# Kernel tuning notes

Hardware: AMD Instinct MI355X
Metric: run time of the kernel (lower is better)

Reference implementation:

```python
import math
import jax, jax.numpy as jnp
import numpy as np

D = 256      # embedding_dim (= internal_dim, downsample_rate 1)
H = 8        # num_heads
HD = D // H  # head_dim = 32
NTC = 16     # num_text_classes
NIMG = 4096  # image tokens (64x64)
N = NIMG + NTC
B = 2
NKE = 64     # num_k_exclude_rope


def _rope(x, freqs):
    # x: (b, h, n, c); freqs: (n, c//2, 2) = (cos, sin) of complex rotary factors
    b, h, n, c = x.shape
    xp = x.reshape(b, h, n, c // 2, 2)
    cos, sin = freqs[..., 0], freqs[..., 1]
    xr, xi = xp[..., 0], xp[..., 1]
    out_r = xr * cos - xi * sin
    out_i = xr * sin + xi * cos
    return jnp.stack([out_r, out_i], axis=-1).reshape(b, h, n, c)


def _sep_heads(x):
    b, n, c = x.shape
    return x.reshape(b, n, H, c // H).transpose(0, 2, 1, 3)  # (b,h,n,hd)


def setup_inputs() -> dict:
    key = jax.random.key(0)
    ks = jax.random.split(key, 14)
    s = 0.02
    # rotary factors: unit-norm cos/sin pairs
    ang_img = jax.random.uniform(ks[3], (NIMG, HD // 2)) * (2.0 * np.pi)
    ang_txt = jax.random.uniform(ks[4], (NTC, HD // 2)) * (2.0 * np.pi)
    return {
        "q": jax.random.normal(ks[0], (B, N, D), dtype=jnp.float32),
        "k": jax.random.normal(ks[1], (B, N, D), dtype=jnp.float32),
        "v": jax.random.normal(ks[2], (B, N, D), dtype=jnp.float32),
        "freqs_cis_img": jnp.stack([jnp.cos(ang_img), jnp.sin(ang_img)], axis=-1),
        "freqs_cis_txt": jnp.stack([jnp.cos(ang_txt), jnp.sin(ang_txt)], axis=-1),
        "Wq": jax.random.normal(ks[5], (D, D), dtype=jnp.float32) * s,
        "bq": jnp.zeros((D,), dtype=jnp.float32),
        "Wk": jax.random.normal(ks[6], (D, D), dtype=jnp.float32) * s,
        "bk": jnp.zeros((D,), dtype=jnp.float32),
        "Wv": jax.random.normal(ks[7], (D, D), dtype=jnp.float32) * s,
        "bv": jnp.zeros((D,), dtype=jnp.float32),
        "Wo": jax.random.normal(ks[8], (D, D), dtype=jnp.float32) * s,
        "bo": jnp.zeros((D,), dtype=jnp.float32),
        "num_k_exclude_rope": NKE,
    }


def reference(q, k, v, freqs_cis_img, freqs_cis_txt,
              Wq, bq, Wk, bk, Wv, bv, Wo, bo, num_k_exclude_rope):
    q = q @ Wq.T + bq
    k = k @ Wk.T + bk
    v = v @ Wv.T + bv
    q = _sep_heads(q)  # (b,h,n,hd)
    k = _sep_heads(k)
    v = _sep_heads(v)

    # split tokens into image / text regions, apply RoPE separately
    q_img, q_txt = q[:, :, :-NTC, :], q[:, :, -NTC:, :]
    k_img, k_txt = k[:, :, :-NTC, :], k[:, :, -NTC:, :]
    q_img = _rope(q_img, freqs_cis_img)
    k_img = _rope(k_img, freqs_cis_img)
    q_txt = _rope(q_txt, freqs_cis_txt)
    k_txt = _rope(k_txt, freqs_cis_txt)
    q = jnp.concatenate([q_img, q_txt], axis=-2)
    k = jnp.concatenate([k_img, k_txt], axis=-2)

    scale = 1.0 / math.sqrt(HD)
    nke = num_k_exclude_rope
    if nke > 0:
        k_td, k_mem = k[:, :, :-nke, :], k[:, :, -nke:, :]
        v_td, v_mem = v[:, :, :-nke, :], v[:, :, -nke:, :]
        attn = jax.nn.softmax(jnp.einsum('bhqd,bhkd->bhqk', q, k_td) * scale, axis=-1)
        out = jnp.einsum('bhqk,bhkd->bhqd', attn, v_td)
        attn_m = jax.nn.softmax(jnp.einsum('bhqd,bhkd->bhqk', q, k_mem) * scale, axis=-1)
        out = out + jnp.einsum('bhqk,bhkd->bhqd', attn_m, v_mem)
    else:
        attn = jax.nn.softmax(jnp.einsum('bhqd,bhkd->bhqk', q, k) * scale, axis=-1)
        out = jnp.einsum('bhqk,bhkd->bhqd', attn, v)

    b, h, n, hd = out.shape
    out = out.transpose(0, 2, 1, 3).reshape(b, n, h * hd)
    return out @ Wo.T + bo
```

## Files before the change

kernel.cpp:

```cpp
#include <hip/hip_runtime.h>
#include <hip/hip_bf16.h>

#define BN    4112
#define NKR   4160
#define BNP   4160
#define BB    2
#define HH    8
#define NIMG_ 4096
#define NMAIN 4048
#define MROWS 8224
#define QSCALE 0.25505402f

typedef __attribute__((ext_vector_type(8))) short short8;
typedef __attribute__((ext_vector_type(4))) float f32x4;

__device__ __forceinline__ unsigned short f2bs(float x) { return __bfloat16_as_ushort(__float2bfloat16(x)); }
__device__ __forceinline__ unsigned pkbf(float a, float b) {
    __hip_bfloat162 h = __float22bfloat162_rn(make_float2(a, b));
    unsigned u; __builtin_memcpy(&u, &h, 4); return u;
}
__device__ __forceinline__ float fexp2(float x) {
#if __has_builtin(__builtin_amdgcn_exp2f)
    return __builtin_amdgcn_exp2f(x);
#else
    return exp2f(x);
#endif
}

__global__ __launch_bounds__(256)
void qkv_mfma(const float* __restrict__ Aq, const float* __restrict__ Ak, const float* __restrict__ Av,
              const float* __restrict__ Wq, const float* __restrict__ Wk, const float* __restrict__ Wv,
              const float* __restrict__ bq, const float* __restrict__ bk, const float* __restrict__ bv,
              short* __restrict__ Qr, short* __restrict__ Kr, short* __restrict__ Vt,
              const float* __restrict__ fimg, const float* __restrict__ ftxt)
{
    __shared__ __align__(16) short Ws[2][64][72];
    __shared__ __align__(16) short Ds[2][64][72];

    const int mode = blockIdx.z;
    const float* A    = (mode == 0) ? Aq : (mode == 1) ? Ak : Av;
    const float* W    = (mode == 0) ? Wq : (mode == 1) ? Wk : Wv;
    const float* bias = (mode == 0) ? bq : (mode == 1) ? bk : bv;

    const int t    = threadIdx.x;
    const int wave = t >> 6, lane = t & 63, q16 = lane & 15, quad = lane >> 4;
    const int f0 = blockIdx.x * 64;
    const int m0 = blockIdx.y * 64;
    const int sr = t >> 2, sc = (t & 3) * 16;
    const int arow = m0 + sr;
    const bool aval = arow < MROWS;
    const float* wp = W + (size_t)(f0 + sr) * 256 + sc;
    const float* ap = A + (size_t)(aval ? arow : 0) * 256 + sc;

    f32x4 acc[4] = {{0,0,0,0},{0,0,0,0},{0,0,0,0},{0,0,0,0}};

    uint4 wr0, wr1, dr0, dr1;
    {
        float4 a0 = *(const float4*)(wp),     a1 = *(const float4*)(wp + 4);
        float4 a2 = *(const float4*)(wp + 8), a3 = *(const float4*)(wp + 12);
        wr0 = uint4{pkbf(a0.x,a0.y), pkbf(a0.z,a0.w), pkbf(a1.x,a1.y), pkbf(a1.z,a1.w)};
        wr1 = uint4{pkbf(a2.x,a2.y), pkbf(a2.z,a2.w), pkbf(a3.x,a3.y), pkbf(a3.z,a3.w)};
        a0 = *(const float4*)(ap);     a1 = *(const float4*)(ap + 4);
        a2 = *(const float4*)(ap + 8); a3 = *(const float4*)(ap + 12);
        dr0 = uint4{pkbf(a0.x,a0.y), pkbf(a0.z,a0.w), pkbf(a1.x,a1.y), pkbf(a1.z,a1.w)};
        dr1 = uint4{pkbf(a2.x,a2.y), pkbf(a2.z,a2.w), pkbf(a3.x,a3.y), pkbf(a3.z,a3.w)};
    }
    *(uint4*)&Ws[0][sr][sc] = wr0; *(uint4*)&Ws[0][sr][sc + 8] = wr1;
    *(uint4*)&Ds[0][sr][sc] = dr0; *(uint4*)&Ds[0][sr][sc + 8] = dr1;
    __syncthreads();

    #pragma unroll
    for (int ki = 0; ki < 4; ++ki) {
        const int buf = ki & 1;
        if (ki < 3) {
            const int k1 = (ki + 1) * 64;
            float4 a0 = *(const float4*)(wp + k1),     a1 = *(const float4*)(wp + k1 + 4);
            float4 a2 = *(const float4*)(wp + k1 + 8), a3 = *(const float4*)(wp + k1 + 12);
            wr0 = uint4{pkbf(a0.x,a0.y), pkbf(a0.z,a0.w), pkbf(a1.x,a1.y), pkbf(a1.z,a1.w)};
            wr1 = uint4{pkbf(a2.x,a2.y), pkbf(a2.z,a2.w), pkbf(a3.x,a3.y), pkbf(a3.z,a3.w)};
            a0 = *(const float4*)(ap + k1);     a1 = *(const float4*)(ap + k1 + 4);
            a2 = *(const float4*)(ap + k1 + 8); a3 = *(const float4*)(ap + k1 + 12);
            dr0 = uint4{pkbf(a0.x,a0.y), pkbf(a0.z,a0.w), pkbf(a1.x,a1.y), pkbf(a1.z,a1.w)};
            dr1 = uint4{pkbf(a2.x,a2.y), pkbf(a2.z,a2.w), pkbf(a3.x,a3.y), pkbf(a3.z,a3.w)};
        }
        #pragma unroll
        for (int ks = 0; ks < 2; ++ks) {
            const short8 af = *(const short8*)&Ws[buf][wave * 16 + q16][ks * 32 + quad * 8];
            #pragma unroll
            for (int ct = 0; ct < 4; ++ct) {
                const short8 bf = *(const short8*)&Ds[buf][ct * 16 + q16][ks * 32 + quad * 8];
                acc[ct] = __builtin_amdgcn_mfma_f32_16x16x32_bf16(af, bf, acc[ct], 0, 0, 0);
            }
        }
        if (ki < 3) {
            *(uint4*)&Ws[buf ^ 1][sr][sc] = wr0; *(uint4*)&Ws[buf ^ 1][sr][sc + 8] = wr1;
            *(uint4*)&Ds[buf ^ 1][sr][sc] = dr0; *(uint4*)&Ds[buf ^ 1][sr][sc + 8] = dr1;
            __syncthreads();
        }
    }

    const int fbase = f0 + wave * 16 + quad * 4;
    const float4 bb = *(const float4*)(bias + fbase);
    float vs[4][4];
    #pragma unroll
    for (int ct = 0; ct < 4; ++ct) {
        int n = m0 + ct * 16 + q16;
        float v0 = acc[ct][0] + bb.x, v1 = acc[ct][1] + bb.y;
        float v2 = acc[ct][2] + bb.z, v3 = acc[ct][3] + bb.w;
        int b  = (n >= BN) ? 1 : 0;
        int nb = n - b * BN;
        if (mode < 2) {
            int j0 = (fbase & 31) >> 1;
            const float* fr = (nb < NIMG_) ? (fimg + ((size_t)nb * 16 + j0) * 2)
                                           : (ftxt + ((size_t)(nb - NIMG_) * 16 + j0) * 2);
            float4 cs = *(const float4*)fr;
            float r0 = v0 * cs.x - v1 * cs.y, i0 = v0 * cs.y + v1 * cs.x;
            float r1 = v2 * cs.z - v3 * cs.w, i1 = v2 * cs.w + v3 * cs.z;
            v0 = r0; v1 = i0; v2 = r1; v3 = i1;
        }
        if (mode == 2) {
            vs[ct][0] = v0; vs[ct][1] = v1; vs[ct][2] = v2; vs[ct][3] = v3;
            continue;
        }
        if (n >= MROWS) continue;
        const int h = (fbase >> 5) & 7, hd = fbase & 31;
        if (mode == 0) {
            unsigned short* op = (unsigned short*)Qr + (((size_t)(b * HH + h) * BN + nb) * 32 + hd);
            *(uint2*)op = uint2{pkbf(v0 * QSCALE, v1 * QSCALE), pkbf(v2 * QSCALE, v3 * QSCALE)};
        } else {
            int nk = nb + ((nb >= NMAIN) ? 48 : 0);
            unsigned short* op = (unsigned short*)Kr + (((size_t)(b * HH + h) * NKR + nk) * 32 + hd);
            *(uint2*)op = uint2{pkbf(v0, v1), pkbf(v2, v3)};
        }
    }

    if (mode == 2) {
        short (*Tr)[72] = Ds[0];
        const int fl = wave * 16 + quad * 4;
        #pragma unroll
        for (int ct = 0; ct < 4; ++ct) {
            const int nl = ct * 16 + q16;
            Tr[fl + 0][nl] = (short)f2bs(vs[ct][0]);
            Tr[fl + 1][nl] = (short)f2bs(vs[ct][1]);
            Tr[fl + 2][nl] = (short)f2bs(vs[ct][2]);
            Tr[fl + 3][nl] = (short)f2bs(vs[ct][3]);
        }
        __syncthreads();
        const int h0 = (f0 >> 5) & 7;
        #pragma unroll
        for (int ii = 0; ii < 2; ++ii) {
            const int r  = ii * 32 + (t >> 3);
            const int c8 = (t & 7) * 8;
            const int ng = m0 + c8;
            if (ng < MROWS) {
                uint4 val = *(const uint4*)&Tr[r][c8];
                int b  = (ng >= BN) ? 1 : 0;
                int nb = ng - b * BN;
                int nk = nb + ((nb >= NMAIN) ? 48 : 0);
                int h  = h0 + (r >> 5), hd = r & 31;
                unsigned short* op = (unsigned short*)Vt + ((size_t)(b * HH + h) * 32 + hd) * BNP + nk;
                *(uint4*)op = val;
            }
        }
    }

    if (blockIdx.x == 0 && blockIdx.y < 16 && t < 192) {
        const int bh = blockIdx.y;
        if (mode == 1) {
            short* base = Kr + (size_t)bh * NKR * 32 + (size_t)NMAIN * 32;
            *(uint4*)(base + t * 8) = uint4{0u, 0u, 0u, 0u};
        } else if (mode == 2) {
            short* base = Vt + (size_t)bh * 32 * BNP + (size_t)(t / 6) * BNP + NMAIN + (t % 6) * 8;
            *(uint4*)base = uint4{0u, 0u, 0u, 0u};
        }
    }
}

__global__ __launch_bounds__(512, 8)
void attn_mfma(const short* __restrict__ Qr, const short* __restrict__ Kr,
               const short* __restrict__ Vt, unsigned short* __restrict__ AO)
{
    __shared__ __align__(16) short Ks[2][2][64][40];
    __shared__ __align__(16) short Vs[2][2][32][72];

    const int t    = threadIdx.x;
    const int wave = t >> 6, lane = t & 63, q16 = lane & 15, quad = lane >> 4;
    const int grp  = wave >> 2, w4 = wave & 3;
    const int bh = blockIdx.y;
    const int q  = blockIdx.x * 64 + w4 * 16 + q16;
    const int qc = (q < BN) ? q : (BN - 1);
    const short8 qf = *(const short8*)(Qr + ((size_t)bh * BN + qc) * 32 + quad * 8);

    f32x4 oA0 = {0,0,0,0}, oA1 = {0,0,0,0}, oB0 = {0,0,0,0}, oB1 = {0,0,0,0};
    float LA = 0.f, LB = 0.f;

    const int tg = t & 255;
    const int kr = tg >> 2, kc = tg & 3;
    const int vr = tg >> 3, vc = tg & 7;
    const short* kg = Kr + (size_t)bh * NKR * 32 + (size_t)grp * 65536 + (size_t)kr * 32 + kc * 8;
    const short* vg = Vt + (size_t)bh * 32 * BNP + (size_t)vr * BNP + grp * 2048
                         + (vc >> 2) * 32 + (vc & 3) * 4;
    const int ntiles = 32 + grp;

    auto tile = [&](int buf, f32x4& o0, f32x4& o1, float& L) {
        float lsum = 0.f;
        #pragma unroll
        for (int g = 0; g < 2; ++g) {
            const short8 kf0 = *(const short8*)&Ks[grp][buf][(2*g)     * 16 + q16][quad * 8];
            const short8 kf1 = *(const short8*)&Ks[grp][buf][(2*g + 1) * 16 + q16][quad * 8];
            f32x4 z = {0,0,0,0};
            f32x4 s0 = __builtin_amdgcn_mfma_f32_16x16x32_bf16(kf0, qf, z, 0, 0, 0);
            f32x4 s1 = __builtin_amdgcn_mfma_f32_16x16x32_bf16(kf1, qf, z, 0, 0, 0);
            float p0 = fexp2(s0[0]), p1 = fexp2(s0[1]), p2 = fexp2(s0[2]), p3 = fexp2(s0[3]);
            float p4 = fexp2(s1[0]), p5 = fexp2(s1[1]), p6 = fexp2(s1[2]), p7 = fexp2(s1[3]);
            lsum += ((p0 + p1) + (p2 + p3)) + ((p4 + p5) + (p6 + p7));
            uint4 pbu = uint4{pkbf(p0, p1), pkbf(p2, p3), pkbf(p4, p5), pkbf(p6, p7)};
            short8 pb; __builtin_memcpy(&pb, &pbu, 16);
            const short8 vf = *(const short8*)&Vs[grp][buf][q16][g * 32 + quad * 8];
            o0 = __builtin_amdgcn_mfma_f32_16x16x32_bf16(vf, pb, o0, 0, 0, 0);
            const short8 vb = *(const short8*)&Vs[grp][buf][16 + q16][g * 32 + quad * 8];
            o1 = __builtin_amdgcn_mfma_f32_16x16x32_bf16(vb, pb, o1, 0, 0, 0);
        }
        L += lsum;
    };

    *(uint4*)&Ks[grp][0][kr][kc * 8] = *(const uint4*)(kg);
    {
        uint2 va = *(const uint2*)(vg);
        uint2 vbr = *(const uint2*)(vg + 16);
        *(uint4*)&Vs[grp][0][vr][vc * 8] = uint4{va.x, va.y, vbr.x, vbr.y};
    }
    __syncthreads();

    for (int it = 0; it < 33; ++it) {
        const int buf = it & 1;
        uint4 kreg; uint2 vreg0, vreg1;
        const bool pre = (it + 1) < ntiles;
        if (pre) {
            kreg  = *(const uint4*)(kg + (size_t)(it + 1) * 2048);
            vreg0 = *(const uint2*)(vg + (it + 1) * 64);
            vreg1 = *(const uint2*)(vg + (it + 1) * 64 + 16);
        }
        if (it < ntiles) {
            if (grp == 0) tile(buf, oA0, oA1, LA);
            else if (it < 32) tile(buf, oA0, oA1, LA);
            else              tile(buf, oB0, oB1, LB);
        }
        if (pre) {
            *(uint4*)&Ks[grp][buf ^ 1][kr][kc * 8] = kreg;
            *(uint4*)&Vs[grp][buf ^ 1][vr][vc * 8] = uint4{vreg0.x, vreg0.y, vreg1.x, vreg1.y};
        }
        __syncthreads();
    }

    LA += __shfl_xor(LA, 16); LA += __shfl_xor(LA, 32);
    LB += __shfl_xor(LB, 16); LB += __shfl_xor(LB, 32);

    float* ex = (float*)&Ks[0][0][0][0];
    const int slot = (w4 * 64 + lane) * 12;
    if (grp == 0) {
        *(f32x4*)(ex + slot)     = oA0;
        *(f32x4*)(ex + slot + 4) = oA1;
        ex[slot + 8] = LA;
    }
    __syncthreads();

    if (grp == 1 && q < BN) {
        f32x4 a0 = *(const f32x4*)(ex + slot);
        f32x4 a1 = *(const f32x4*)(ex + slot + 4);
        float LT = LA + ex[slot + 8] - 48.f;
        const float iA = 1.f / LT, iB = 1.f / LB;
        const int b = bh >> 3, h = bh & 7;
        unsigned short* ap = AO + ((size_t)b * BN + q) * 256 + h * 32;
        float w0[4], w1[4];
        #pragma unroll
        for (int r = 0; r < 4; ++r) {
            w0[r] = (oA0[r] + a0[r]) * iA + oB0[r] * iB;
            w1[r] = (oA1[r] + a1[r]) * iA + oB1[r] * iB;
        }
        *(uint2*)(ap + quad * 4)      = uint2{pkbf(w0[0], w0[1]), pkbf(w0[2], w0[3])};
        *(uint2*)(ap + 16 + quad * 4) = uint2{pkbf(w1[0], w1[1]), pkbf(w1[2], w1[3])};
    }
}

__global__ __launch_bounds__(256)
void gemm_out(const unsigned short* __restrict__ A, const float* __restrict__ W,
              const float* __restrict__ bias, float* __restrict__ out)
{
    __shared__ __align__(16) short Ws[2][64][72];
    __shared__ __align__(16) short Ds[2][64][72];
    const int t    = threadIdx.x;
    const int wave = t >> 6, lane = t & 63, q16 = lane & 15, quad = lane >> 4;
    const int f0 = blockIdx.x * 64, m0 = blockIdx.y * 64;
    const int sr = t >> 2, sc = (t & 3) * 16;
    const int arow = m0 + sr;
    const bool aval = arow < MROWS;
    const float* wp = W + (size_t)(f0 + sr) * 256 + sc;
    const unsigned short* ap = A + (size_t)(aval ? arow : 0) * 256 + sc;

    f32x4 acc[4] = {{0,0,0,0},{0,0,0,0},{0,0,0,0},{0,0,0,0}};

    uint4 wr0, wr1, dr0, dr1;
    {
        float4 a0 = *(const float4*)(wp),     a1 = *(const float4*)(wp + 4);
        float4 a2 = *(const float4*)(wp + 8), a3 = *(const float4*)(wp + 12);
        wr0 = uint4{pkbf(a0.x,a0.y), pkbf(a0.z,a0.w), pkbf(a1.x,a1.y), pkbf(a1.z,a1.w)};
        wr1 = uint4{pkbf(a2.x,a2.y), pkbf(a2.z,a2.w), pkbf(a3.x,a3.y), pkbf(a3.z,a3.w)};
        dr0 = *(const uint4*)(ap); dr1 = *(const uint4*)(ap + 8);
    }
    *(uint4*)&Ws[0][sr][sc] = wr0; *(uint4*)&Ws[0][sr][sc + 8] = wr1;
    *(uint4*)&Ds[0][sr][sc] = dr0; *(uint4*)&Ds[0][sr][sc + 8] = dr1;
    __syncthreads();

    #pragma unroll
    for (int ki = 0; ki < 4; ++ki) {
        const int buf = ki & 1;
        if (ki < 3) {
            const int k1 = (ki + 1) * 64;
            float4 a0 = *(const float4*)(wp + k1),     a1 = *(const float4*)(wp + k1 + 4);
            float4 a2 = *(const float4*)(wp + k1 + 8), a3 = *(const float4*)(wp + k1 + 12);
            wr0 = uint4{pkbf(a0.x,a0.y), pkbf(a0.z,a0.w), pkbf(a1.x,a1.y), pkbf(a1.z,a1.w)};
            wr1 = uint4{pkbf(a2.x,a2.y), pkbf(a2.z,a2.w), pkbf(a3.x,a3.y), pkbf(a3.z,a3.w)};
            dr0 = *(const uint4*)(ap + k1); dr1 = *(const uint4*)(ap + k1 + 8);
        }
        #pragma unroll
        for (int ks = 0; ks < 2; ++ks) {
            const short8 af = *(const short8*)&Ws[buf][wave * 16 + q16][ks * 32 + quad * 8];
            #pragma unroll
            for (int ct = 0; ct < 4; ++ct) {
                const short8 bf = *(const short8*)&Ds[buf][ct * 16 + q16][ks * 32 + quad * 8];
                acc[ct] = __builtin_amdgcn_mfma_f32_16x16x32_bf16(af, bf, acc[ct], 0, 0, 0);
            }
        }
        if (ki < 3) {
            *(uint4*)&Ws[buf ^ 1][sr][sc] = wr0; *(uint4*)&Ws[buf ^ 1][sr][sc + 8] = wr1;
            *(uint4*)&Ds[buf ^ 1][sr][sc] = dr0; *(uint4*)&Ds[buf ^ 1][sr][sc + 8] = dr1;
            __syncthreads();
        }
    }

    const int fbase = f0 + wave * 16 + quad * 4;
    const float4 bb = *(const float4*)(bias + fbase);
    #pragma unroll
    for (int ct = 0; ct < 4; ++ct) {
        int n = m0 + ct * 16 + q16;
        if (n >= MROWS) continue;
        float* op = out + (size_t)n * 256 + fbase;
        *(float4*)op = float4{acc[ct][0] + bb.x, acc[ct][1] + bb.y,
                              acc[ct][2] + bb.z, acc[ct][3] + bb.w};
    }
}

extern "C" void kernel_launch(void* const* d_in, const int* in_sizes, int n_in,
                              void* d_out, int out_size, void* d_ws, size_t ws_size,
                              hipStream_t stream)
{
    (void)in_sizes; (void)n_in; (void)out_size; (void)ws_size;
    const float* q    = (const float*)d_in[0];
    const float* k    = (const float*)d_in[1];
    const float* v    = (const float*)d_in[2];
    const float* fimg = (const float*)d_in[3];
    const float* ftxt = (const float*)d_in[4];
    const float* Wq   = (const float*)d_in[5];
    const float* bq   = (const float*)d_in[6];
    const float* Wk   = (const float*)d_in[7];
    const float* bk   = (const float*)d_in[8];
    const float* Wv   = (const float*)d_in[9];
    const float* bv   = (const float*)d_in[10];
    const float* Wo   = (const float*)d_in[11];
    const float* bo   = (const float*)d_in[12];

    char* w = (char*)d_ws;
    short*          Qr = (short*)(w);
    short*          Kr = (short*)(w + 4210688);
    short*          Vt = (short*)(w + 8470528);
    unsigned short* AO = (unsigned short*)(w + 12730368);

    qkv_mfma<<<dim3(4, 129, 3), 256, 0, stream>>>(q, k, v, Wq, Wk, Wv, bq, bk, bv,
                                                  Qr, Kr, Vt, fimg, ftxt);
    attn_mfma<<<dim3(65, 16), 512, 0, stream>>>(Qr, Kr, Vt, AO);
    gemm_out<<<dim3(4, 129), 256, 0, stream>>>(AO, Wo, bo, (float*)d_out);
}
```

Before: 202.7 us.

## Switch attention to 32x32x16 MFMA with 128 queries per block

The attention kernel now uses 32x32x16 bf16 MFMA instead of 16x16x32. Each wave handles 32 queries, so a block covers 128 queries and the grid halves from 65 to 33 blocks along the query axis. The V staging layout, the lane mapping of the reductions, the cross-group merge slots and the output writes are all remapped to the 32x32 accumulator layout, and the MFMA/exp section is wrapped in s_setprio. The goal is to reuse each K/V tile over more queries and to cut instruction overhead per FLOP. In exchange, register pressure rises (launch bounds relaxed from 8 to 4 blocks) and fewer blocks are available for parallelism.

After: 205.4 us. No clear change (+1.3%).

```diff
diff --git a/kernel.cpp b/kernel.cpp
--- a/kernel.cpp
+++ b/kernel.cpp
@@ -13,6 +13,7 @@
 
 typedef __attribute__((ext_vector_type(8))) short short8;
 typedef __attribute__((ext_vector_type(4))) float f32x4;
+typedef __attribute__((ext_vector_type(16))) float f32x16;
 
 __device__ __forceinline__ unsigned short f2bs(float x) { return __bfloat16_as_ushort(__float2bfloat16(x)); }
 __device__ __forceinline__ unsigned pkbf(float a, float b) {
@@ -176,7 +177,7 @@
     }
 }
 
-__global__ __launch_bounds__(512, 8)
+__global__ __launch_bounds__(512, 4)
 void attn_mfma(const short* __restrict__ Qr, const short* __restrict__ Kr,
                const short* __restrict__ Vt, unsigned short* __restrict__ AO)
 {
@@ -184,14 +185,18 @@
     __shared__ __align__(16) short Vs[2][2][32][72];
 
     const int t    = threadIdx.x;
-    const int wave = t >> 6, lane = t & 63, q16 = lane & 15, quad = lane >> 4;
+    const int wave = t >> 6, lane = t & 63, q32 = lane & 31, hi = lane >> 5;
     const int grp  = wave >> 2, w4 = wave & 3;
     const int bh = blockIdx.y;
-    const int q  = blockIdx.x * 64 + w4 * 16 + q16;
+    const int q  = blockIdx.x * 128 + w4 * 32 + q32;
     const int qc = (q < BN) ? q : (BN - 1);
-    const short8 qf = *(const short8*)(Qr + ((size_t)bh * BN + qc) * 32 + quad * 8);
-
-    f32x4 oA0 = {0,0,0,0}, oA1 = {0,0,0,0}, oB0 = {0,0,0,0}, oB1 = {0,0,0,0};
+    const short* qp = Qr + ((size_t)bh * BN + qc) * 32 + hi * 8;
+    const short8 qf0 = *(const short8*)(qp);
+    const short8 qf1 = *(const short8*)(qp + 16);
+
+    f32x16 oA = {0,0,0,0,0,0,0,0,0,0,0,0,0,0,0,0};
+    f32x16 oB = {0,0,0,0,0,0,0,0,0,0,0,0,0,0,0,0};
+    const f32x16 z16 = {0,0,0,0,0,0,0,0,0,0,0,0,0,0,0,0};
     float LA = 0.f, LB = 0.f;
 
     const int tg = t & 255;
@@ -199,27 +204,30 @@
     const int vr = tg >> 3, vc = tg & 7;
     const short* kg = Kr + (size_t)bh * NKR * 32 + (size_t)grp * 65536 + (size_t)kr * 32 + kc * 8;
     const short* vg = Vt + (size_t)bh * 32 * BNP + (size_t)vr * BNP + grp * 2048
-                         + (vc >> 2) * 32 + (vc & 3) * 4;
+                         + (vc >> 1) * 16 + (vc & 1) * 4;
     const int ntiles = 32 + grp;
 
-    auto tile = [&](int buf, f32x4& o0, f32x4& o1, float& L) {
+    auto tile = [&](int buf, f32x16& o, float& L) {
         float lsum = 0.f;
         #pragma unroll
-        for (int g = 0; g < 2; ++g) {
-            const short8 kf0 = *(const short8*)&Ks[grp][buf][(2*g)     * 16 + q16][quad * 8];
-            const short8 kf1 = *(const short8*)&Ks[grp][buf][(2*g + 1) * 16 + q16][quad * 8];
-            f32x4 z = {0,0,0,0};
-            f32x4 s0 = __builtin_amdgcn_mfma_f32_16x16x32_bf16(kf0, qf, z, 0, 0, 0);
-            f32x4 s1 = __builtin_amdgcn_mfma_f32_16x16x32_bf16(kf1, qf, z, 0, 0, 0);
-            float p0 = fexp2(s0[0]), p1 = fexp2(s0[1]), p2 = fexp2(s0[2]), p3 = fexp2(s0[3]);
-            float p4 = fexp2(s1[0]), p5 = fexp2(s1[1]), p6 = fexp2(s1[2]), p7 = fexp2(s1[3]);
-            lsum += ((p0 + p1) + (p2 + p3)) + ((p4 + p5) + (p6 + p7));
-            uint4 pbu = uint4{pkbf(p0, p1), pkbf(p2, p3), pkbf(p4, p5), pkbf(p6, p7)};
-            short8 pb; __builtin_memcpy(&pb, &pbu, 16);
-            const short8 vf = *(const short8*)&Vs[grp][buf][q16][g * 32 + quad * 8];
-            o0 = __builtin_amdgcn_mfma_f32_16x16x32_bf16(vf, pb, o0, 0, 0, 0);
-            const short8 vb = *(const short8*)&Vs[grp][buf][16 + q16][g * 32 + quad * 8];
-            o1 = __builtin_amdgcn_mfma_f32_16x16x32_bf16(vb, pb, o1, 0, 0, 0);
+        for (int h = 0; h < 2; ++h) {
+            const short8 kf0 = *(const short8*)&Ks[grp][buf][h * 32 + q32][hi * 8];
+            const short8 kf1 = *(const short8*)&Ks[grp][buf][h * 32 + q32][16 + hi * 8];
+            f32x16 s = __builtin_amdgcn_mfma_f32_32x32x16_bf16(kf0, qf0, z16, 0, 0, 0);
+            s = __builtin_amdgcn_mfma_f32_32x32x16_bf16(kf1, qf1, s, 0, 0, 0);
+            float p[16];
+            #pragma unroll
+            for (int r = 0; r < 16; ++r) p[r] = fexp2(s[r]);
+            lsum += (((p[0]+p[1])+(p[2]+p[3])) + ((p[4]+p[5])+(p[6]+p[7])))
+                  + (((p[8]+p[9])+(p[10]+p[11])) + ((p[12]+p[13])+(p[14]+p[15])));
+            #pragma unroll
+            for (int m = 0; m < 2; ++m) {
+                uint4 pbu = uint4{pkbf(p[8*m+0], p[8*m+1]), pkbf(p[8*m+2], p[8*m+3]),
+                                  pkbf(p[8*m+4], p[8*m+5]), pkbf(p[8*m+6], p[8*m+7])};
+                short8 pb; __builtin_memcpy(&pb, &pbu, 16);
+                const short8 vf = *(const short8*)&Vs[grp][buf][q32][h * 32 + m * 16 + hi * 8];
+                o = __builtin_amdgcn_mfma_f32_32x32x16_bf16(vf, pb, o, 0, 0, 0);
+            }
         }
         L += lsum;
     };
@@ -227,8 +235,8 @@
     *(uint4*)&Ks[grp][0][kr][kc * 8] = *(const uint4*)(kg);
     {
         uint2 va = *(const uint2*)(vg);
-        uint2 vbr = *(const uint2*)(vg + 16);
-        *(uint4*)&Vs[grp][0][vr][vc * 8] = uint4{va.x, va.y, vbr.x, vbr.y};
+        uint2 vb = *(const uint2*)(vg + 8);
+        *(uint4*)&Vs[grp][0][vr][vc * 8] = uint4{va.x, va.y, vb.x, vb.y};
     }
     __syncthreads();
 
@@ -239,12 +247,14 @@
         if (pre) {
             kreg  = *(const uint4*)(kg + (size_t)(it + 1) * 2048);
             vreg0 = *(const uint2*)(vg + (it + 1) * 64);
-            vreg1 = *(const uint2*)(vg + (it + 1) * 64 + 16);
+            vreg1 = *(const uint2*)(vg + (it + 1) * 64 + 8);
         }
         if (it < ntiles) {
-            if (grp == 0) tile(buf, oA0, oA1, LA);
-            else if (it < 32) tile(buf, oA0, oA1, LA);
-            else              tile(buf, oB0, oB1, LB);
+            __builtin_amdgcn_s_setprio(1);
+            if (grp == 0)      tile(buf, oA, LA);
+            else if (it < 32)  tile(buf, oA, LA);
+            else               tile(buf, oB, LB);
+            __builtin_amdgcn_s_setprio(0);
         }
         if (pre) {
             *(uint4*)&Ks[grp][buf ^ 1][kr][kc * 8] = kreg;
@@ -253,33 +263,33 @@
         __syncthreads();
     }
 
-    LA += __shfl_xor(LA, 16); LA += __shfl_xor(LA, 32);
-    LB += __shfl_xor(LB, 16); LB += __shfl_xor(LB, 32);
+    LA += __shfl_xor(LA, 32);
+    LB += __shfl_xor(LB, 32);
 
     float* ex = (float*)&Ks[0][0][0][0];
-    const int slot = (w4 * 64 + lane) * 12;
+    const int slot = (w4 * 64 + lane) * 20;
     if (grp == 0) {
-        *(f32x4*)(ex + slot)     = oA0;
-        *(f32x4*)(ex + slot + 4) = oA1;
-        ex[slot + 8] = LA;
+        #pragma unroll
+        for (int i = 0; i < 4; ++i)
+            *(f32x4*)(ex + slot + 4 * i) = f32x4{oA[4*i], oA[4*i+1], oA[4*i+2], oA[4*i+3]};
+        ex[slot + 16] = LA;
     }
     __syncthreads();
 
     if (grp == 1 && q < BN) {
-        f32x4 a0 = *(const f32x4*)(ex + slot);
-        f32x4 a1 = *(const f32x4*)(ex + slot + 4);
-        float LT = LA + ex[slot + 8] - 48.f;
+        float LT = LA + ex[slot + 16] - 48.f;
         const float iA = 1.f / LT, iB = 1.f / LB;
         const int b = bh >> 3, h = bh & 7;
         unsigned short* ap = AO + ((size_t)b * BN + q) * 256 + h * 32;
-        float w0[4], w1[4];
-        #pragma unroll
-        for (int r = 0; r < 4; ++r) {
-            w0[r] = (oA0[r] + a0[r]) * iA + oB0[r] * iB;
-            w1[r] = (oA1[r] + a1[r]) * iA + oB1[r] * iB;
-        }
-        *(uint2*)(ap + quad * 4)      = uint2{pkbf(w0[0], w0[1]), pkbf(w0[2], w0[3])};
-        *(uint2*)(ap + 16 + quad * 4) = uint2{pkbf(w1[0], w1[1]), pkbf(w1[2], w1[3])};
+        #pragma unroll
+        for (int k = 0; k < 4; ++k) {
+            f32x4 a = *(const f32x4*)(ex + slot + 4 * k);
+            float w0 = (oA[4*k+0] + a[0]) * iA + oB[4*k+0] * iB;
+            float w1 = (oA[4*k+1] + a[1]) * iA + oB[4*k+1] * iB;
+            float w2 = (oA[4*k+2] + a[2]) * iA + oB[4*k+2] * iB;
+            float w3 = (oA[4*k+3] + a[3]) * iA + oB[4*k+3] * iB;
+            *(uint2*)(ap + 8 * k + 4 * hi) = uint2{pkbf(w0, w1), pkbf(w2, w3)};
+        }
     }
 }
 
@@ -378,6 +388,6 @@
 
     qkv_mfma<<<dim3(4, 129, 3), 256, 0, stream>>>(q, k, v, Wq, Wk, Wv, bq, bk, bv,
                                                   Qr, Kr, Vt, fimg, ftxt);
-    attn_mfma<<<dim3(65, 16), 512, 0, stream>>>(Qr, Kr, Vt, AO);
+    attn_mfma<<<dim3(33, 16), 512, 0, stream>>>(Qr, Kr, Vt, AO);
     gemm_out<<<dim3(4, 129), 256, 0, stream>>>(AO, Wo, bo, (float*)d_out);
 }
```
